# Optimization experiments

Measured on AMD Instinct MI355X. Metric: run time of the kernel, lower is better.

## Reference

```python
import jax, jax.numpy as jnp
import numpy as np

T, B, S = 32, 64, 64      # tgt_len, batch, src_len
E, H, V = 512, 1024, 32000  # embed, hidden, vocab
LE, NL = 32, 4            # lang embed size, num languages
SCALE = 0.02


def setup_inputs() -> dict:
    key = jax.random.key(0)
    ks = jax.random.split(key, 20)
    r = lambda k, shp: SCALE * jax.random.normal(k, shp, dtype=jnp.float32)
    return {
        "x": jax.random.randint(ks[0], (T, B), 0, V),
        "src_lengths": jax.random.randint(ks[1], (B,), 1, S + 1),
        "lang_idx": 0,
        "h0": jax.random.normal(ks[2], (1, B, H), dtype=jnp.float32),
        "c0": jax.random.normal(ks[3], (1, B, H), dtype=jnp.float32),
        "src_encodings": jax.random.normal(ks[4], (S, B, H), dtype=jnp.float32),
        "vocab_embed": r(ks[5], (V, E)),
        "lang_embed": r(ks[6], (NL, LE)),
        "W_wih": r(ks[7], (4 * H * E, LE)), "b_wih": r(ks[8], (4 * H * E,)),
        "W_whh": r(ks[9], (4 * H * H, LE)), "b_whh": r(ks[10], (4 * H * H,)),
        "W_bih": r(ks[11], (4 * H, LE)), "b_bih": r(ks[12], (4 * H,)),
        "W_bhh": r(ks[13], (4 * H, LE)), "b_bhh": r(ks[14], (4 * H,)),
        "c2h_W": r(ks[15], (H, 2 * H)), "c2h_b": r(ks[16], (H,)),
        "h2o_W": r(ks[17], (V, H)), "h2o_b": r(ks[18], (V,)),
    }


def reference(x, src_lengths, lang_idx, h0, c0, src_encodings,
              vocab_embed, lang_embed,
              W_wih, b_wih, W_whh, b_whh, W_bih, b_bih, W_bhh, b_bhh,
              c2h_W, c2h_b, h2o_W, h2o_b):
    hdim = c0.shape[-1]
    emb = vocab_embed[x]                       # (T,B,E)
    el = lang_embed[lang_idx]                  # (LE,)
    # hypernetwork generates the LSTM cell weights for this language
    w_ih = (W_wih @ el + b_wih).reshape(4 * hdim, -1)   # (4H,E)
    w_hh = (W_whh @ el + b_whh).reshape(4 * hdim, hdim)  # (4H,H)
    b_ih = W_bih @ el + b_bih                  # (4H,)
    b_hh = W_bhh @ el + b_bhh

    def step(carry, xt):
        h, c = carry
        gates = xt @ w_ih.T + h @ w_hh.T + b_ih + b_hh
        i, f, g, o = jnp.split(gates, 4, axis=-1)
        c = jax.nn.sigmoid(f) * c + jax.nn.sigmoid(i) * jnp.tanh(g)
        h = jax.nn.sigmoid(o) * jnp.tanh(c)
        return (h, c), h

    (hN, cN), rnn_out = jax.lax.scan(step, (h0[0], c0[0]), emb)  # rnn_out (T,B,H)

    # Luong dot attention with source-length masking
    scores = jnp.einsum('tbh,sbh->tbs', rnn_out, src_encodings)
    mask = jnp.arange(src_encodings.shape[0])[None, :] < src_lengths[:, None]  # (B,S)
    scores = jnp.where(mask[None], scores, jnp.float32(-1e30))
    attn = jax.nn.softmax(scores, axis=-1)
    context = jnp.einsum('tbs,sbh->tbh', attn, src_encodings)

    concat = jnp.concatenate([context, rnn_out], axis=-1)   # (T,B,2H)
    attn_hidden = jnp.tanh(concat @ c2h_W.T + c2h_b)         # (T,B,H)
    output = attn_hidden @ h2o_W.T + h2o_b                   # (T,B,V)
    return output, hN[None], cN[None]
```

## Files before the change

### kernel.cpp

```cpp
#include <hip/hip_runtime.h>
#include <math.h>

#define Tt 32
#define Bb 64
#define Ss 64
#define Ee 512
#define Hh 1024
#define Vv 32000
#define LEc 32
#define G4H 4096
#define Mm 2048

typedef __bf16 bf16x8 __attribute__((ext_vector_type(8)));
typedef float f32x4 __attribute__((ext_vector_type(4)));
typedef short short4v __attribute__((ext_vector_type(4)));

__device__ __forceinline__ short f2bf(float f){
  unsigned u = __builtin_bit_cast(unsigned, f);
  u += 0x7fffu + ((u >> 16) & 1u);
  return (short)(u >> 16);
}

__device__ __forceinline__ void gl_lds16(const short* g, short* l){
  __builtin_amdgcn_global_load_lds((const __attribute__((address_space(1))) void*)g,
                                   (__attribute__((address_space(3))) void*)l, 16, 0, 0);
}

__global__ __launch_bounds__(256) void k_prep(
    const float* __restrict__ Wih, const float* __restrict__ bihv,
    const float* __restrict__ Whh, const float* __restrict__ bhhv,
    const float* __restrict__ Wbih, const float* __restrict__ bbih,
    const float* __restrict__ Wbhh, const float* __restrict__ bbhh,
    const float* __restrict__ lang_embed, const int* __restrict__ lang_idx,
    const int* __restrict__ x, const float* __restrict__ vocab,
    const float* __restrict__ h0, const float* __restrict__ c0,
    short* __restrict__ w_ih, short* __restrict__ w_hh, float* __restrict__ b_total,
    short* __restrict__ emb, short* __restrict__ hbf, float* __restrict__ c)
{
  int blk = blockIdx.x;
  if (blk < 24576){
    const long NIH = (long)G4H * Ee;
    long r = (long)blk * 256 + threadIdx.x;
    const float4* el4 = (const float4*)(lang_embed + (size_t)lang_idx[0] * LEc);
    float4 e[8];
    #pragma unroll
    for (int j = 0; j < 8; j++) e[j] = el4[j];
    const float4* W4; float bb; short* outp;
    if (r < NIH){ W4 = (const float4*)(Wih + r * LEc); bb = bihv[r]; outp = w_ih + r; }
    else { long rr = r - NIH; W4 = (const float4*)(Whh + rr * LEc); bb = bhhv[rr]; outp = w_hh + rr; }
    float acc = bb;
    #pragma unroll
    for (int j = 0; j < 8; j++){
      float4 w = W4[j];
      acc += w.x*e[j].x + w.y*e[j].y + w.z*e[j].z + w.w*e[j].w;
    }
    *outp = f2bf(acc);
  } else if (blk < 24592){
    int u = (blk - 24576) * 256 + threadIdx.x;
    const float* el = lang_embed + (size_t)lang_idx[0] * LEc;
    float acc = bbih[u] + bbhh[u];
    #pragma unroll
    for (int j = 0; j < LEc; j++)
      acc += (Wbih[(size_t)u*LEc + j] + Wbhh[(size_t)u*LEc + j]) * el[j];
    b_total[u] = acc;
  } else if (blk < 25616){
    int tid = (blk - 24592) * 256 + threadIdx.x;
    int row = tid / (Ee / 4);
    int j4 = (tid % (Ee / 4)) * 4;
    int tok = x[row];
    float4 v = *(const float4*)(vocab + (size_t)tok * Ee + j4);
    short4v o = { f2bf(v.x), f2bf(v.y), f2bf(v.z), f2bf(v.w) };
    *(short4v*)(emb + (size_t)row * Ee + j4) = o;
  } else {
    int i = (blk - 25616) * 256 + threadIdx.x;
    hbf[i] = f2bf(h0[i]);
    c[i] = c0[i];
  }
}

template<int M, int N, int K, int MODE>
__global__ __launch_bounds__(256) void k_gemm(
    const short* __restrict__ A, const short* __restrict__ B,
    const float* __restrict__ bias, void* __restrict__ Cv)
{
  __shared__ short lA[4096];
  __shared__ short lB[4096];
  const int nwg = (M/128)*(N/128);
  int xcd = blockIdx.x & 7, pos = blockIdx.x >> 3;
  int wg = xcd * (nwg >> 3) + pos;
  const int MT = M/128;
  int mt = wg % MT;
  int nt = wg / MT;

  int t = threadIdx.x;
  int wave = t >> 6, lane = t & 63;
  int wm = wave >> 1, wn = wave & 1;
  int tr = t >> 2;
  int tc = (t & 3) * 8;

  const short* Agp = A + (size_t)(mt*128)*K;
  const short* Bgp = B + (size_t)(nt*128)*K;

  f32x4 acc[4][4];
  #pragma unroll
  for (int i = 0; i < 4; i++)
    #pragma unroll
    for (int j = 0; j < 4; j++) acc[i][j] = (f32x4){0.f,0.f,0.f,0.f};

  int ra = lane & 15, ko = (lane >> 4) * 8;

  for (int k0 = 0; k0 < K; k0 += 32){
    #pragma unroll
    for (int q2 = 0; q2 < 2; q2++){
      gl_lds16(Agp + (size_t)(q2*64 + tr)*K + k0 + tc, &lA[q2*2048 + wave*512]);
      gl_lds16(Bgp + (size_t)(q2*64 + tr)*K + k0 + tc, &lB[q2*2048 + wave*512]);
    }
    __syncthreads();
    bf16x8 av[4], bv[4];
    #pragma unroll
    for (int i = 0; i < 4; i++){
      av[i] = *(const bf16x8*)&lA[(wm*64 + i*16 + ra)*32 + ko];
      bv[i] = *(const bf16x8*)&lB[(wn*64 + i*16 + ra)*32 + ko];
    }
    #pragma unroll
    for (int i = 0; i < 4; i++)
      #pragma unroll
      for (int j = 0; j < 4; j++)
        acc[i][j] = __builtin_amdgcn_mfma_f32_16x16x32_bf16(av[i], bv[j], acc[i][j], 0, 0, 0);
    __syncthreads();
  }

  int col = lane & 15, r0 = (lane >> 4) * 4;
  #pragma unroll
  for (int i = 0; i < 4; i++)
    #pragma unroll
    for (int j = 0; j < 4; j++)
      #pragma unroll
      for (int q = 0; q < 4; q++){
        int m = mt*128 + wm*64 + i*16 + r0 + q;
        int n = nt*128 + wn*64 + j*16 + col;
        float v = acc[i][j][q] + bias[n];
        if (MODE == 0) ((float*)Cv)[(size_t)m * N + n] = v;
        else           ((short*)Cv)[(size_t)m * N + n] = f2bf(tanhf(v));
      }
}

#define VMW4 asm volatile("s_waitcnt vmcnt(4)" ::: "memory")
#define VMW0 asm volatile("s_waitcnt vmcnt(0)" ::: "memory")
#define VMNONE ((void)0)

#define PHASE(d, lp, LOADB, VMW, ...) do { \
    bf16x8 afr[2][2]; \
    _Pragma("unroll") \
    for (int ii = 0; ii < 2; ii++){ \
      _Pragma("unroll") \
      for (int ks = 0; ks < 2; ks++){ \
        int r = (2*(lp)+ii)*16 + la15; \
        int sc = (ks*4 + l4) ^ (r & 7); \
        afr[ii][ks] = *(const bf16x8*)(lds + ((d)*2+wm)*16384 + (r*8+sc)*16); \
      } \
    } \
    if (LOADB){ \
      _Pragma("unroll") \
      for (int fj = 0; fj < 4; fj++){ \
        _Pragma("unroll") \
        for (int ks = 0; ks < 2; ks++){ \
          int grow = wn*64 + fj*16 + la15; \
          int hh = grow >> 7, rb = grow & 127; \
          int sc = (ks*4 + l4) ^ (rb & 7); \
          bfr[fj][ks] = *(const bf16x8*)(lds + 65536 + ((d)*2+hh)*16384 + (rb*8+sc)*16); \
        } \
      } \
    } \
    __VA_ARGS__; \
    __builtin_amdgcn_s_barrier(); \
    asm volatile("s_waitcnt lgkmcnt(0)" ::: "memory"); \
    __builtin_amdgcn_sched_barrier(0); \
    __builtin_amdgcn_s_setprio(1); \
    _Pragma("unroll") \
    for (int ii = 0; ii < 2; ii++){ \
      _Pragma("unroll") \
      for (int ks = 0; ks < 2; ks++){ \
        _Pragma("unroll") \
        for (int fj = 0; fj < 4; fj++){ \
          acc[2*(lp)+ii][fj] = __builtin_amdgcn_mfma_f32_16x16x32_bf16(afr[ii][ks], bfr[fj][ks], acc[2*(lp)+ii][fj], 0, 0, 0); \
        } \
      } \
    } \
    __builtin_amdgcn_s_setprio(0); \
    VMW; \
    __builtin_amdgcn_s_barrier(); \
  } while (0)

__global__ __launch_bounds__(512, 2) void k_h2o8(
    const short* __restrict__ A, const short* __restrict__ Bw,
    const float* __restrict__ bias, float* __restrict__ C)
{
  extern __shared__ char lds[];
  int tid = threadIdx.x;
  int wave = tid >> 6, lane = tid & 63;
  int wm = wave >> 2, wn = wave & 3;
  int la15 = lane & 15, l4 = lane >> 4;
  int col = lane & 15, r0 = (lane >> 4) * 4;

  int nt  = blockIdx.x >> 1;
  int mtb = (blockIdx.x & 1) * 4;
  const short* Bg = Bw + (size_t)(nt*256)*Hh;

  for (int tp = 0; tp < 4; tp++){
    int mt = mtb + tp;
    const short* Ag = A + (size_t)(mt*256)*Hh;

    auto stage_half = [&](const short* G, int Xoff, int d, int h, int kt){
      #pragma unroll
      for (int call = 0; call < 2; call++){
        int chunk = call*512 + tid;
        int rr = chunk >> 3;
        int cc = (chunk & 7) ^ (rr & 7);
        const short* src = G + (size_t)(h*128 + rr)*Hh + kt*64 + cc*8;
        char* dst = lds + Xoff + (d*2+h)*16384 + call*8192 + wave*1024;
        gl_lds16(src, (short*)dst);
      }
    };

    f32x4 acc[8][4];
    #pragma unroll
    for (int i = 0; i < 8; i++)
      #pragma unroll
      for (int j = 0; j < 4; j++) acc[i][j] = (f32x4){0.f,0.f,0.f,0.f};
    bf16x8 bfr[4][2];

    stage_half(Ag, 0,     0, 0, 0); stage_half(Ag, 0,     0, 1, 0);
    stage_half(Bg, 65536, 0, 0, 0); stage_half(Bg, 65536, 0, 1, 0);
    stage_half(Bg, 65536, 1, 0, 1); stage_half(Bg, 65536, 1, 1, 1);
    VMW4;
    __builtin_amdgcn_s_barrier();

    for (int it = 0; it < 7; it++){
      int kt0 = 2*it;
      PHASE(0, 0, true,  VMNONE, stage_half(Ag, 0,     1, 0, kt0+1));
      PHASE(0, 1, false, VMNONE, stage_half(Ag, 0,     1, 1, kt0+1));
      PHASE(0, 2, false, VMNONE, stage_half(Bg, 65536, 0, 0, kt0+2));
      PHASE(0, 3, false, VMW4,   stage_half(Bg, 65536, 0, 1, kt0+2));
      PHASE(1, 0, true,  VMNONE, stage_half(Ag, 0,     0, 0, kt0+2));
      PHASE(1, 1, false, VMNONE, stage_half(Ag, 0,     0, 1, kt0+2));
      PHASE(1, 2, false, VMNONE, stage_half(Bg, 65536, 1, 0, kt0+3));
      PHASE(1, 3, false, VMW4,   stage_half(Bg, 65536, 1, 1, kt0+3));
    }
    PHASE(0, 0, true,  VMNONE, stage_half(Ag, 0, 1, 0, 15));
    PHASE(0, 1, false, VMNONE, stage_half(Ag, 0, 1, 1, 15));
    PHASE(0, 2, false, VMNONE, VMNONE);
    PHASE(0, 3, false, VMW0,   VMNONE);
    PHASE(1, 0, true,  VMNONE, VMNONE);
    PHASE(1, 1, false, VMNONE, VMNONE);
    PHASE(1, 2, false, VMNONE, VMNONE);
    PHASE(1, 3, false, VMNONE, VMNONE);

    #pragma unroll
    for (int fi = 0; fi < 8; fi++)
      #pragma unroll
      for (int fj = 0; fj < 4; fj++)
        #pragma unroll
        for (int q = 0; q < 4; q++){
          int m = mt*256 + wm*128 + fi*16 + r0 + q;
          int n = nt*256 + wn*64 + fj*16 + col;
          C[(size_t)m * Vv + n] = acc[fi][fj][q] + bias[n];
        }
  }
}

#define PIG4 8716288L
#define PIGQ 272384L
#define H2O4 8192000L
__global__ __launch_bounds__(256) void k_step(
    int t, const short* __restrict__ h_in, const short* __restrict__ w_hh,
    const float* __restrict__ Gx, float* __restrict__ c,
    short* __restrict__ h_out, float* __restrict__ rnn_out, short* __restrict__ concat,
    const float* __restrict__ h2oW, short* __restrict__ h2oWb,
    const float* __restrict__ c2hW, short* __restrict__ c2hWb)
{
  if (blockIdx.x >= 256){
    long pb = blockIdx.x - 256;
    long base = (long)t * PIGQ;
    for (long i = pb*256 + threadIdx.x; i < PIGQ; i += 65536){
      long gi = base + i;
      const float* src; short* dst;
      if (gi < H2O4){ src = h2oW + gi*4; dst = h2oWb + gi*4; }
      else { long j = gi - H2O4; src = c2hW + j*4; dst = c2hWb + j*4; }
      float4 v = *(const float4*)src;
      short4v o = { f2bf(v.x), f2bf(v.y), f2bf(v.z), f2bf(v.w) };
      *(short4v*)dst = o;
    }
    return;
  }
  __shared__ float red[4][4][16][16];
  int mt = blockIdx.x >> 6;
  int n0 = (blockIdx.x & 63) * 16;
  int wv = threadIdx.x >> 6;
  int lane = threadIdx.x & 63;
  int ra = lane & 15, ko = (lane >> 4) * 8;
  f32x4 acc[4] = {{0,0,0,0},{0,0,0,0},{0,0,0,0},{0,0,0,0}};
  const short* Ap = h_in + (size_t)(mt*16 + ra) * Hh + wv*256 + ko;
  const short* Bp = w_hh + (size_t)(n0    + ra) * Hh + wv*256 + ko;
  #pragma unroll
  for (int kk = 0; kk < 256; kk += 32){
    bf16x8 a = *(const bf16x8*)(Ap + kk);
    #pragma unroll
    for (int g = 0; g < 4; g++){
      bf16x8 b = *(const bf16x8*)(Bp + (size_t)g*Hh*Hh + kk);
      acc[g] = __builtin_amdgcn_mfma_f32_16x16x32_bf16(a, b, acc[g], 0, 0, 0);
    }
  }
  int col = lane & 15, r0 = (lane >> 4) * 4;
  #pragma unroll
  for (int g = 0; g < 4; g++)
    #pragma unroll
    for (int i = 0; i < 4; i++)
      red[wv][g][r0 + i][col] = acc[g][i];
  __syncthreads();

  int r  = threadIdx.x >> 4;
  int cc = threadIdx.x & 15;
  int b  = mt*16 + r;
  int u  = n0 + cc;
  float gate[4];
  #pragma unroll
  for (int g = 0; g < 4; g++){
    float s = Gx[((size_t)t*Bb + b) * G4H + g*Hh + u];
    #pragma unroll
    for (int w2 = 0; w2 < 4; w2++) s += red[w2][g][r][cc];
    gate[g] = s;
  }
  float ig = 1.f / (1.f + expf(-gate[0]));
  float fg = 1.f / (1.f + expf(-gate[1]));
  float gg = tanhf(gate[2]);
  float og = 1.f / (1.f + expf(-gate[3]));
  size_t bu = (size_t)b * Hh + u;
  float cn = fg * c[bu] + ig * gg;
  c[bu] = cn;
  float hn = og * tanhf(cn);
  h_out[bu] = f2bf(hn);
  size_t row = (size_t)t * Bb + b;
  rnn_out[row * Hh + u] = hn;
  concat[row * (2*Hh) + Hh + u] = f2bf(hn);
}

__global__ __launch_bounds__(256) void k_attn(
    const float* __restrict__ rnn_out, const float* __restrict__ src,
    const int* __restrict__ src_len, short* __restrict__ concat,
    const float* __restrict__ cbuf, float* __restrict__ out)
{
  if (blockIdx.x >= 256){
    int pb = blockIdx.x - 256;
    for (int i = pb*256 + threadIdx.x; i < Bb*Hh; i += 1024){
      out[(size_t)Mm * Vv + i]           = rnn_out[(size_t)(Tt-1)*Bb*Hh + i];
      out[(size_t)Mm * Vv + Bb*Hh + i]   = cbuf[i];
    }
    return;
  }
  __shared__ float srcL[64 * 129];
  __shared__ float rnnL[8 * 129];
  __shared__ float satt[8][64];

  int b  = blockIdx.x & 63;
  int t0 = (blockIdx.x >> 6) * 8;
  int tid = threadIdx.x;
  int wave = tid >> 6, lane = tid & 63;

  float sc0 = 0.f, sc1 = 0.f;
  for (int c0 = 0; c0 < Hh; c0 += 128){
    __syncthreads();
    for (int i = tid; i < 64*128; i += 256){
      int s = i >> 7, h = i & 127;
      srcL[s*129 + h] = src[((size_t)s*Bb + b) * Hh + c0 + h];
    }
    for (int i = tid; i < 8*128; i += 256){
      int rr = i >> 7, h = i & 127;
      rnnL[rr*129 + h] = rnn_out[((size_t)(t0+rr)*Bb + b) * Hh + c0 + h];
    }
    __syncthreads();
    const float* sp = &srcL[lane*129];
    const float* r0p = &rnnL[(2*wave)*129];
    const float* r1p = &rnnL[(2*wave+1)*129];
    #pragma unroll 8
    for (int h = 0; h < 128; h++){
      float sv = sp[h];
      sc0 += r0p[h] * sv;
      sc1 += r1p[h] * sv;
    }
  }
  int slen = src_len[b];
  if (lane >= slen){ sc0 = -1e30f; sc1 = -1e30f; }
  float mx0 = sc0, mx1 = sc1;
  for (int o = 32; o; o >>= 1){ mx0 = fmaxf(mx0, __shfl_xor(mx0, o, 64)); mx1 = fmaxf(mx1, __shfl_xor(mx1, o, 64)); }
  float p0 = expf(sc0 - mx0), p1 = expf(sc1 - mx1);
  float s0 = p0, s1 = p1;
  for (int o = 32; o; o >>= 1){ s0 += __shfl_xor(s0, o, 64); s1 += __shfl_xor(s1, o, 64); }
  satt[2*wave][lane]   = p0 / s0;
  satt[2*wave+1][lane] = p1 / s1;
  __syncthreads();

  int h0 = tid * 4;
  float4 acc[8];
  #pragma unroll
  for (int i = 0; i < 8; i++) acc[i] = make_float4(0.f, 0.f, 0.f, 0.f);
  for (int s = 0; s < Ss; s++){
    float4 sv = *(const float4*)(src + ((size_t)s*Bb + b) * Hh + h0);
    #pragma unroll
    for (int i = 0; i < 8; i++){
      float a = satt[i][s];
      acc[i].x += a*sv.x; acc[i].y += a*sv.y; acc[i].z += a*sv.z; acc[i].w += a*sv.w;
    }
  }
  #pragma unroll
  for (int i = 0; i < 8; i++){
    size_t row = (size_t)(t0 + i)*Bb + b;
    short4v o = { f2bf(acc[i].x), f2bf(acc[i].y), f2bf(acc[i].z), f2bf(acc[i].w) };
    *(short4v*)(concat + row * (2*Hh) + h0) = o;
  }
}

extern "C" void kernel_launch(void* const* d_in, const int* in_sizes, int n_in,
                              void* d_out, int out_size, void* d_ws, size_t ws_size,
                              hipStream_t stream) {
  const int*   x         = (const int*)  d_in[0];
  const int*   src_len   = (const int*)  d_in[1];
  const int*   lang_idx  = (const int*)  d_in[2];
  const float* h0        = (const float*)d_in[3];
  const float* c0        = (const float*)d_in[4];
  const float* src       = (const float*)d_in[5];
  const float* vocab     = (const float*)d_in[6];
  const float* lang_emb  = (const float*)d_in[7];
  const float* Wih       = (const float*)d_in[8];
  const float* bih       = (const float*)d_in[9];
  const float* Whh       = (const float*)d_in[10];
  const float* bhh       = (const float*)d_in[11];
  const float* Wbih      = (const float*)d_in[12];
  const float* bbih      = (const float*)d_in[13];
  const float* Wbhh      = (const float*)d_in[14];
  const float* bbhh      = (const float*)d_in[15];
  const float* c2hW      = (const float*)d_in[16];
  const float* c2hb      = (const float*)d_in[17];
  const float* h2oW      = (const float*)d_in[18];
  const float* h2ob      = (const float*)d_in[19];
  float* out = (float*)d_out;

  char* ws = (char*)d_ws;
  short* w_ih   = (short*)(ws + 0);
  short* w_hh   = (short*)(ws + 4194304);
  short* c2hWb  = (short*)(ws + 12582912);
  short* h2oWb  = (short*)(ws + 16777216);
  float* b_tot  = (float*)(ws + 82313216);
  short* emb    = (short*)(ws + 82329600);
  float* Gx     = (float*)(ws + 84426752);
  short* hb0    = (short*)(ws + 117981184);
  short* hb1    = (short*)(ws + 118112256);
  float* cbuf   = (float*)(ws + 118243328);
  float* rnn    = (float*)(ws + 118505472);
  short* concat = (short*)(ws + 126894080);
  short* ah     = (short*)(ws + 135806976);

  k_prep<<<25872, 256, 0, stream>>>(Wih, bih, Whh, bhh, Wbih, bbih, Wbhh, bbhh,
                                    lang_emb, lang_idx, x, vocab, h0, c0,
                                    w_ih, w_hh, b_tot, emb, hb0, cbuf);

  k_gemm<Mm, G4H, Ee, 0><<<(Mm/128)*(G4H/128), 256, 0, stream>>>(emb, w_ih, b_tot, Gx);

  short* hbuf[2] = { hb0, hb1 };
  for (int t = 0; t < Tt; t++){
    k_step<<<512, 256, 0, stream>>>(t, hbuf[t & 1], w_hh, Gx, cbuf,
                                    hbuf[(t + 1) & 1], rnn, concat,
                                    h2oW, h2oWb, c2hW, c2hWb);
  }

  k_attn<<<260, 256, 0, stream>>>(rnn, src, src_len, concat, cbuf, out);

  k_gemm<Mm, Hh, 2*Hh, 1><<<(Mm/128)*(Hh/128), 256, 0, stream>>>(concat, c2hWb, c2hb, ah);
  hipFuncSetAttribute((const void*)k_h2o8, hipFuncAttributeMaxDynamicSharedMemorySize, 131072);
  k_h2o8<<<250, 512, 131072, stream>>>(ah, h2oWb, h2ob, out);
}
```

Before: 724.4 us.

## Overlap w_hh hypernetwork generation with input-gate GEMM in one launch

The w_hh hypernetwork projection moves out of the prep kernel into extra blocks of a new combined kernel that also runs the input-to-gates GEMM. The bandwidth-heavy weight generation can then run alongside the compute-bound MFMA GEMM instead of serially before it. The step kernel's block-to-tile mapping is also remapped so consecutive column tiles land on the same XCD, which should improve L2 locality for w_hh. The cost is a duplicated GEMM body and contention between the two block types for CUs and memory bandwidth.

```diff
diff --git a/kernel.cpp b/kernel.cpp
--- a/kernel.cpp
+++ b/kernel.cpp
@@ -28,43 +28,39 @@
 
 __global__ __launch_bounds__(256) void k_prep(
     const float* __restrict__ Wih, const float* __restrict__ bihv,
-    const float* __restrict__ Whh, const float* __restrict__ bhhv,
     const float* __restrict__ Wbih, const float* __restrict__ bbih,
     const float* __restrict__ Wbhh, const float* __restrict__ bbhh,
     const float* __restrict__ lang_embed, const int* __restrict__ lang_idx,
     const int* __restrict__ x, const float* __restrict__ vocab,
     const float* __restrict__ h0, const float* __restrict__ c0,
-    short* __restrict__ w_ih, short* __restrict__ w_hh, float* __restrict__ b_total,
+    short* __restrict__ w_ih, float* __restrict__ b_total,
     short* __restrict__ emb, short* __restrict__ hbf, float* __restrict__ c)
 {
   int blk = blockIdx.x;
-  if (blk < 24576){
-    const long NIH = (long)G4H * Ee;
+  if (blk < 8192){
     long r = (long)blk * 256 + threadIdx.x;
     const float4* el4 = (const float4*)(lang_embed + (size_t)lang_idx[0] * LEc);
     float4 e[8];
     #pragma unroll
     for (int j = 0; j < 8; j++) e[j] = el4[j];
-    const float4* W4; float bb; short* outp;
-    if (r < NIH){ W4 = (const float4*)(Wih + r * LEc); bb = bihv[r]; outp = w_ih + r; }
-    else { long rr = r - NIH; W4 = (const float4*)(Whh + rr * LEc); bb = bhhv[rr]; outp = w_hh + rr; }
-    float acc = bb;
+    const float4* W4 = (const float4*)(Wih + r * LEc);
+    float acc = bihv[r];
     #pragma unroll
     for (int j = 0; j < 8; j++){
       float4 w = W4[j];
       acc += w.x*e[j].x + w.y*e[j].y + w.z*e[j].z + w.w*e[j].w;
     }
-    *outp = f2bf(acc);
-  } else if (blk < 24592){
-    int u = (blk - 24576) * 256 + threadIdx.x;
+    w_ih[r] = f2bf(acc);
+  } else if (blk < 8208){
+    int u = (blk - 8192) * 256 + threadIdx.x;
     const float* el = lang_embed + (size_t)lang_idx[0] * LEc;
     float acc = bbih[u] + bbhh[u];
     #pragma unroll
     for (int j = 0; j < LEc; j++)
       acc += (Wbih[(size_t)u*LEc + j] + Wbhh[(size_t)u*LEc + j]) * el[j];
     b_total[u] = acc;
-  } else if (blk < 25616){
-    int tid = (blk - 24592) * 256 + threadIdx.x;
+  } else if (blk < 9232){
+    int tid = (blk - 8208) * 256 + threadIdx.x;
     int row = tid / (Ee / 4);
     int j4 = (tid % (Ee / 4)) * 4;
     int tok = x[row];
@@ -72,10 +68,98 @@
     short4v o = { f2bf(v.x), f2bf(v.y), f2bf(v.z), f2bf(v.w) };
     *(short4v*)(emb + (size_t)row * Ee + j4) = o;
   } else {
-    int i = (blk - 25616) * 256 + threadIdx.x;
+    int i = (blk - 9232) * 256 + threadIdx.x;
     hbf[i] = f2bf(h0[i]);
     c[i] = c0[i];
   }
+}
+
+__global__ __launch_bounds__(256) void k_xgates_pig(
+    const short* __restrict__ A, const short* __restrict__ B,
+    const float* __restrict__ bias, float* __restrict__ Gx,
+    const float* __restrict__ Whh, const float* __restrict__ bhhv,
+    const float* __restrict__ lang_embed, const int* __restrict__ lang_idx,
+    short* __restrict__ w_hh)
+{
+  if (blockIdx.x >= 512){
+    long pb = blockIdx.x - 512;
+    const float4* el4 = (const float4*)(lang_embed + (size_t)lang_idx[0] * LEc);
+    float4 e[8];
+    #pragma unroll
+    for (int j = 0; j < 8; j++) e[j] = el4[j];
+    #pragma unroll 2
+    for (int it = 0; it < 8; it++){
+      long r = pb*2048 + it*256 + threadIdx.x;
+      const float4* W4 = (const float4*)(Whh + r * LEc);
+      float acc = bhhv[r];
+      #pragma unroll
+      for (int j = 0; j < 8; j++){
+        float4 w = W4[j];
+        acc += w.x*e[j].x + w.y*e[j].y + w.z*e[j].z + w.w*e[j].w;
+      }
+      w_hh[r] = f2bf(acc);
+    }
+    return;
+  }
+  const int M = Mm, N = G4H, K = Ee;
+  __shared__ short lA[4096];
+  __shared__ short lB[4096];
+  const int nwg = 512;
+  int xcd = blockIdx.x & 7, pos = blockIdx.x >> 3;
+  int wg = xcd * (nwg >> 3) + pos;
+  const int MT = M/128;
+  int mt = wg % MT;
+  int nt = wg / MT;
+
+  int t = threadIdx.x;
+  int wave = t >> 6, lane = t & 63;
+  int wm = wave >> 1, wn = wave & 1;
+  int tr = t >> 2;
+  int tc = (t & 3) * 8;
+
+  const short* Agp = A + (size_t)(mt*128)*K;
+  const short* Bgp = B + (size_t)(nt*128)*K;
+
+  f32x4 acc[4][4];
+  #pragma unroll
+  for (int i = 0; i < 4; i++)
+    #pragma unroll
+    for (int j = 0; j < 4; j++) acc[i][j] = (f32x4){0.f,0.f,0.f,0.f};
+
+  int ra = lane & 15, ko = (lane >> 4) * 8;
+
+  for (int k0 = 0; k0 < K; k0 += 32){
+    #pragma unroll
+    for (int q2 = 0; q2 < 2; q2++){
+      gl_lds16(Agp + (size_t)(q2*64 + tr)*K + k0 + tc, &lA[q2*2048 + wave*512]);
+      gl_lds16(Bgp + (size_t)(q2*64 + tr)*K + k0 + tc, &lB[q2*2048 + wave*512]);
+    }
+    __syncthreads();
+    bf16x8 av[4], bv[4];
+    #pragma unroll
+    for (int i = 0; i < 4; i++){
+      av[i] = *(const bf16x8*)&lA[(wm*64 + i*16 + ra)*32 + ko];
+      bv[i] = *(const bf16x8*)&lB[(wn*64 + i*16 + ra)*32 + ko];
+    }
+    #pragma unroll
+    for (int i = 0; i < 4; i++)
+      #pragma unroll
+      for (int j = 0; j < 4; j++)
+        acc[i][j] = __builtin_amdgcn_mfma_f32_16x16x32_bf16(av[i], bv[j], acc[i][j], 0, 0, 0);
+    __syncthreads();
+  }
+
+  int col = lane & 15, r0 = (lane >> 4) * 4;
+  #pragma unroll
+  for (int i = 0; i < 4; i++)
+    #pragma unroll
+    for (int j = 0; j < 4; j++)
+      #pragma unroll
+      for (int q = 0; q < 4; q++){
+        int m = mt*128 + wm*64 + i*16 + r0 + q;
+        int n = nt*128 + wn*64 + j*16 + col;
+        Gx[(size_t)m * N + n] = acc[i][j][q] + bias[n];
+      }
 }
 
 template<int M, int N, int K, int MODE>
@@ -294,8 +378,10 @@
     return;
   }
   __shared__ float red[4][4][16][16];
-  int mt = blockIdx.x >> 6;
-  int n0 = (blockIdx.x & 63) * 16;
+  int xcd = blockIdx.x & 7;
+  int q   = blockIdx.x >> 3;
+  int mt  = q >> 3;
+  int n0  = (xcd * 8 + (q & 7)) * 16;
   int wv = threadIdx.x >> 6;
   int lane = threadIdx.x & 63;
   int ra = lane & 15, ko = (lane >> 4) * 8;
@@ -460,11 +546,12 @@
   short* concat = (short*)(ws + 126894080);
   short* ah     = (short*)(ws + 135806976);
 
-  k_prep<<<25872, 256, 0, stream>>>(Wih, bih, Whh, bhh, Wbih, bbih, Wbhh, bbhh,
-                                    lang_emb, lang_idx, x, vocab, h0, c0,
-                                    w_ih, w_hh, b_tot, emb, hb0, cbuf);
-
-  k_gemm<Mm, G4H, Ee, 0><<<(Mm/128)*(G4H/128), 256, 0, stream>>>(emb, w_ih, b_tot, Gx);
+  k_prep<<<9488, 256, 0, stream>>>(Wih, bih, Wbih, bbih, Wbhh, bbhh,
+                                   lang_emb, lang_idx, x, vocab, h0, c0,
+                                   w_ih, b_tot, emb, hb0, cbuf);
+
+  k_xgates_pig<<<2560, 256, 0, stream>>>(emb, w_ih, b_tot, Gx,
+                                         Whh, bhh, lang_emb, lang_idx, w_hh);
 
   short* hbuf[2] = { hb0, hb1 };
   for (int t = 0; t < Tt; t++){
```

After: 735.5 us. No clear change (+1.5%).
